# Optimization experiments

Measured on AMD Instinct MI355X. Metric: run time of the kernel, lower is better.

## Reference

```python
import jax, jax.numpy as jnp
import numpy as np

C, PE, L, HEADS = 256, 64, 6, 4
N_GRAPHS, S = 2048, 64            # uniform graphs of S nodes -> dense batch is a reshape
N = N_GRAPHS * S                  # 131072 nodes
E = N * 4                         # 524288 edges
BN_EPS = 1e-5


def _bn(h, g, b):
    # BatchNorm1d, training-mode statistics (biased variance), affine
    m = h.mean(0)
    v = h.var(0)
    return (h - m) / jnp.sqrt(v + BN_EPS) * g + b


def setup_inputs() -> dict:
    key = jax.random.key(0)
    ks = iter(jax.random.split(key, 64))
    def rn(shape, scale=0.05):
        return jax.random.normal(next(ks), shape, dtype=jnp.float32) * scale
    x = jax.random.randint(next(ks), (N, 1), 0, 28)
    pe = jax.random.normal(next(ks), (N, 20), dtype=jnp.float32)
    epg = E // N_GRAPHS
    base = (jnp.arange(E) // epg) * S          # edges stay within their graph
    src = base + jax.random.randint(next(ks), (E,), 0, S)
    dst = base + jax.random.randint(next(ks), (E,), 0, S)
    edge_index = jnp.stack([src, dst])
    edge_attr = jax.random.randint(next(ks), (E,), 0, 4)
    batch = jnp.arange(N) // S
    return dict(
        x=x, pe=pe, edge_index=edge_index, edge_attr=edge_attr, batch=batch,
        node_emb=rn((28, C - PE), 1.0), pe_lin_w=rn((20, PE)), pe_lin_b=jnp.zeros(PE),
        pe_norm_g=jnp.ones(20), pe_norm_b=jnp.zeros(20),
        edge_emb=rn((4, C), 1.0),
        conv_w1=rn((L, C, C)), conv_b1=jnp.zeros((L, C)),
        conv_w2=rn((L, C, C)), conv_b2=jnp.zeros((L, C)),
        attn_in_w=rn((L, C, 3 * C)), attn_in_b=jnp.zeros((L, 3 * C)),
        attn_out_w=rn((L, C, C)), attn_out_b=jnp.zeros((L, C)),
        bn1_g=jnp.ones((L, C)), bn1_b=jnp.zeros((L, C)),
        bn2_g=jnp.ones((L, C)), bn2_b=jnp.zeros((L, C)),
        bn3_g=jnp.ones((L, C)), bn3_b=jnp.zeros((L, C)),
        mlp_w1=rn((L, C, 2 * C)), mlp_b1=jnp.zeros((L, 2 * C)),
        mlp_w2=rn((L, 2 * C, C)), mlp_b2=jnp.zeros((L, C)),
        head_w1=rn((C, C // 2)), head_b1=jnp.zeros(C // 2),
        head_w2=rn((C // 2, C // 4)), head_b2=jnp.zeros(C // 4),
        head_w3=rn((C // 4, 1)), head_b3=jnp.zeros(1),
    )


def reference(x, pe, edge_index, edge_attr, batch, node_emb, pe_lin_w, pe_lin_b,
              pe_norm_g, pe_norm_b, edge_emb, conv_w1, conv_b1, conv_w2, conv_b2,
              attn_in_w, attn_in_b, attn_out_w, attn_out_b,
              bn1_g, bn1_b, bn2_g, bn2_b, bn3_g, bn3_b,
              mlp_w1, mlp_b1, mlp_w2, mlp_b2,
              head_w1, head_b1, head_w2, head_b2, head_w3, head_b3):
    x_pe = _bn(pe, pe_norm_g, pe_norm_b)
    h = jnp.concatenate([node_emb[x[:, 0]], x_pe @ pe_lin_w + pe_lin_b], axis=1)  # [N, C]
    ea = edge_emb[edge_attr]                                                      # [E, C]
    src, dst = edge_index[0], edge_index[1]
    d = C // HEADS
    scale = 1.0 / jnp.sqrt(jnp.float32(d))
    for l in range(L):
        # --- local GINEConv: nn((1+eps)*x_i + sum_j relu(x_j + e_ij)), eps=0 ---
        msg = jax.nn.relu(h[src] + ea)                          # gather + add + relu
        aggr = jax.ops.segment_sum(msg, dst, num_segments=N)    # scatter-add
        z = h + aggr
        hl = jax.nn.relu(z @ conv_w1[l] + conv_b1[l]) @ conv_w2[l] + conv_b2[l]
        hl = _bn(hl + h, bn1_g[l], bn1_b[l])                    # residual + norm1
        # --- global multihead attention on dense batch [G, S, C] ---
        hd = h.reshape(N_GRAPHS, S, C)
        qkv = hd @ attn_in_w[l] + attn_in_b[l]
        q, k, v = jnp.split(qkv, 3, axis=-1)
        q = q.reshape(N_GRAPHS, S, HEADS, d).transpose(0, 2, 1, 3)
        k = k.reshape(N_GRAPHS, S, HEADS, d).transpose(0, 2, 1, 3)
        v = v.reshape(N_GRAPHS, S, HEADS, d).transpose(0, 2, 1, 3)
        a = jax.nn.softmax(jnp.einsum('ghqd,ghkd->ghqk', q, k) * scale, axis=-1)
        o = jnp.einsum('ghqk,ghkd->ghqd', a, v).transpose(0, 2, 1, 3).reshape(N_GRAPHS, S, C)
        o = (o @ attn_out_w[l] + attn_out_b[l]).reshape(N, C)
        ha = _bn(o + h, bn2_g[l], bn2_b[l])                     # residual + norm2
        # --- combine + FFN ---
        out = hl + ha
        ff = jax.nn.relu(out @ mlp_w1[l] + mlp_b1[l]) @ mlp_w2[l] + mlp_b2[l]
        h = _bn(out + ff, bn3_g[l], bn3_b[l])                   # residual + norm3
    pooled = jax.ops.segment_sum(h, batch, num_segments=N_GRAPHS)  # global_add_pool -> [G, C]
    t = jax.nn.relu(pooled @ head_w1 + head_b1)
    t = jax.nn.relu(t @ head_w2 + head_b2)
    return t @ head_w3 + head_b3                                   # [G, 1]
```

## Files before the change

kernel.cpp:

```cpp
#include <hip/hip_runtime.h>

#define N_NODES 131072
#define N_EDGES 524288
#define CCH 256
#define N_GRAPHS_ 2048
#define SEQ 64
#define LAYERS 6

typedef unsigned short US;
typedef __attribute__((ext_vector_type(8))) short v8s;
typedef __attribute__((ext_vector_type(8))) unsigned short v8us;
typedef __attribute__((ext_vector_type(4))) float v4f;

__device__ __forceinline__ float b2f(US u) { return __uint_as_float(((unsigned)u) << 16); }
__device__ __forceinline__ US f2b(float f) {
    unsigned u = __float_as_uint(f);
    return (US)((u + 0x7fff + ((u >> 16) & 1)) >> 16);
}
__device__ __forceinline__ void gload16(const US* g, US* l) {
    __builtin_amdgcn_global_load_lds(
        (const __attribute__((address_space(1))) unsigned int*)g,
        (__attribute__((address_space(3))) unsigned int*)l, 16, 0, 0);
}

__device__ float g_stats[512];
__device__ float g_aff1[512];
__device__ float g_aff2[512];
__device__ float g_aff3[512];
__device__ float g_pe[40];
__device__ float g_peaff[40];
__device__ US    g_wt[6 * 655360];
__device__ int   g_csr[N_EDGES];
__device__ int   g_off[N_GRAPHS_ * 65];

__global__ __launch_bounds__(256) void wt_k(const float* __restrict__ cw1, const float* __restrict__ cw2,
                                            const float* __restrict__ aiw, const float* __restrict__ aow,
                                            const float* __restrict__ mw1, const float* __restrict__ mw2) {
    __shared__ float t[64][65];
    int b = blockIdx.x;
    int l = b / 160, r = b % 160;
    const float* src; int ldw, ldk, ctiles; size_t doff;
    if (r < 16)      { src = cw1 + (size_t)l * 65536;  ldw = 256; ldk = 256; ctiles = 4;  doff = 0;      }
    else if (r < 32) { src = cw2 + (size_t)l * 65536;  ldw = 256; ldk = 256; ctiles = 4;  doff = 65536;  r -= 16; }
    else if (r < 80) { src = aiw + (size_t)l * 196608; ldw = 768; ldk = 256; ctiles = 12; doff = 131072; r -= 32; }
    else if (r < 96) { src = aow + (size_t)l * 65536;  ldw = 256; ldk = 256; ctiles = 4;  doff = 327680; r -= 80; }
    else if (r < 128){ src = mw1 + (size_t)l * 131072; ldw = 512; ldk = 256; ctiles = 8;  doff = 393216; r -= 96; }
    else             { src = mw2 + (size_t)l * 131072; ldw = 256; ldk = 512; ctiles = 4;  doff = 524288; r -= 128; }
    int kt = r / ctiles, ct = r % ctiles;
    int k0 = kt * 64, c0 = ct * 64;
    US* dst = g_wt + (size_t)l * 655360 + doff;
    int tid = threadIdx.x;
    int rr = tid >> 4, c4 = (tid & 15) * 4;
    #pragma unroll
    for (int j = 0; j < 4; j++) {
        float4 v = *(const float4*)(src + (size_t)(k0 + rr + j * 16) * ldw + c0 + c4);
        t[rr + j * 16][c4 + 0] = v.x; t[rr + j * 16][c4 + 1] = v.y;
        t[rr + j * 16][c4 + 2] = v.z; t[rr + j * 16][c4 + 3] = v.w;
    }
    __syncthreads();
    #pragma unroll
    for (int j = 0; j < 4; j++) {
        int crow = rr + j * 16;
        ushort4 o;
        o.x = f2b(t[c4 + 0][crow]); o.y = f2b(t[c4 + 1][crow]);
        o.z = f2b(t[c4 + 2][crow]); o.w = f2b(t[c4 + 3][crow]);
        *(ushort4*)(dst + (size_t)(c0 + crow) * ldk + k0 + c4) = o;
    }
}

__global__ __launch_bounds__(256) void csr_k(const int* __restrict__ ei,
                                             const int* __restrict__ attr) {
    __shared__ int deg[64], off[65];
    int g = blockIdx.x, tid = threadIdx.x;
    if (tid < 64) deg[tid] = 0;
    __syncthreads();
    int e = g * 256 + tid;
    int d = ei[N_EDGES + e] - g * 64;
    int slot = atomicAdd(&deg[d], 1);
    __syncthreads();
    if (tid == 0) {
        off[0] = 0;
        for (int i = 0; i < 64; i++) off[i + 1] = off[i] + deg[i];
    }
    __syncthreads();
    g_csr[g * 256 + off[d] + slot] = (ei[e] - g * 64) | (attr[e] << 6);
    if (tid < 65) g_off[g * 65 + tid] = off[tid];
}

__global__ __launch_bounds__(256) void pe_part_k(const float* __restrict__ pe) {
    __shared__ float red[240], red2[240];
    int b = blockIdx.x, tid = threadIdx.x;
    float s = 0.f, s2 = 0.f;
    if (tid < 240) {
        int ch = tid % 20, sub = tid / 20;
        size_t r0 = (size_t)b * 512;
        for (int r = sub; r < 512; r += 12) {
            float v = pe[(r0 + r) * 20 + ch];
            s += v; s2 += v * v;
        }
        red[tid] = s; red2[tid] = s2;
    }
    __syncthreads();
    if (tid < 20) {
        float ts = 0.f, ts2 = 0.f;
        #pragma unroll
        for (int sub = 0; sub < 12; sub++) { ts += red[sub * 20 + tid]; ts2 += red2[sub * 20 + tid]; }
        atomicAdd(&g_pe[tid], ts);
        atomicAdd(&g_pe[20 + tid], ts2);
    }
}

__global__ __launch_bounds__(64) void pe_fin_k(const float* __restrict__ g,
                                               const float* __restrict__ b) {
    int t = threadIdx.x;
    if (t < 20) {
        float mean = g_pe[t] / (float)N_NODES;
        float var  = g_pe[20 + t] / (float)N_NODES - mean * mean;
        float a = g[t] * rsqrtf(var + 1e-5f);
        g_peaff[t] = a;
        g_peaff[20 + t] = b[t] - mean * a;
        g_pe[t] = 0.f;
        g_pe[20 + t] = 0.f;
    }
}

__global__ __launch_bounds__(256) void embed_k(const int* __restrict__ x,
                                               const float* __restrict__ pe,
                                               const float* __restrict__ node_emb,
                                               const float* __restrict__ plw,
                                               const float* __restrict__ plb,
                                               US* __restrict__ h) {
    int n = blockIdx.x;
    int tid = threadIdx.x;
    int xi = x[n];
    float v;
    if (tid < 192) {
        v = node_emb[xi * 192 + tid];
    } else {
        int j = tid - 192;
        float s = plb[j];
        #pragma unroll
        for (int k = 0; k < 20; k++) {
            float p = pe[(size_t)n * 20 + k] * g_peaff[k] + g_peaff[20 + k];
            s += p * plw[k * 64 + j];
        }
        v = s;
    }
    h[(size_t)n * CCH + tid] = f2b(v);
}

__global__ __launch_bounds__(256) void aggr_z_k(const US* __restrict__ h,
                                                const float* __restrict__ eemb,
                                                US* __restrict__ z) {
    __shared__ US ht[64 * 264];
    __shared__ float em[4 * 260];
    __shared__ int off[65], ce[256];
    int g = blockIdx.x, tid = threadIdx.x;
    for (int v = tid; v < 2048; v += 256) {
        int row = v >> 5, seg = (v & 31) * 8;
        *(v8us*)&ht[row * 264 + seg] = *(const v8us*)(h + (size_t)(g * 64 + row) * 256 + seg);
    }
    for (int i = tid; i < 1024; i += 256)
        em[(i >> 8) * 260 + (i & 255)] = eemb[(i >> 8) * 256 + (i & 255)];
    ce[tid] = g_csr[g * 256 + tid];
    if (tid < 65) off[tid] = g_off[g * 65 + tid];
    __syncthreads();

    int dst = tid >> 2, cq = (tid & 3) * 4;
    float acc[64];
    #pragma unroll
    for (int i = 0; i < 64; i++) acc[i] = 0.f;
    int e1 = off[dst + 1];
    for (int e = off[dst]; e < e1; e++) {
        int val = ce[e];
        int src = val & 63, a = (val >> 6) & 3;
        #pragma unroll
        for (int i = 0; i < 16; i++) {
            int c = cq + i * 16;
            ushort4 hv = *(ushort4*)&ht[src * 264 + c];
            float4 ev = *(float4*)&em[a * 260 + c];
            acc[i * 4 + 0] += fmaxf(b2f(hv.x) + ev.x, 0.f);
            acc[i * 4 + 1] += fmaxf(b2f(hv.y) + ev.y, 0.f);
            acc[i * 4 + 2] += fmaxf(b2f(hv.z) + ev.z, 0.f);
            acc[i * 4 + 3] += fmaxf(b2f(hv.w) + ev.w, 0.f);
        }
    }
    US* zp = z + (size_t)(g * 64 + dst) * 256;
    #pragma unroll
    for (int i = 0; i < 16; i++) {
        int c = cq + i * 16;
        ushort4 hv = *(ushort4*)&ht[dst * 264 + c];
        ushort4 o;
        o.x = f2b(b2f(hv.x) + acc[i * 4 + 0]);
        o.y = f2b(b2f(hv.y) + acc[i * 4 + 1]);
        o.z = f2b(b2f(hv.z) + acc[i * 4 + 2]);
        o.w = f2b(b2f(hv.w) + acc[i * 4 + 3]);
        *(ushort4*)(zp + c) = o;
    }
}

template<int NG, bool STATS>
__global__ __launch_bounds__(256, 4) void gemm_mfma_k(const US* __restrict__ A,
                                                      size_t woff, int ldk,
                                                      int w0, int w1, int w2, int w3,
                                                      const float* __restrict__ bias,
                                                      const US* __restrict__ res,
                                                      US* __restrict__ Y, int mode) {
    const US* __restrict__ Wt = g_wt + woff;
    __shared__ __align__(16) char smem[8192 + 2 * NG * 4096];
    US* As0 = (US*)smem;
    US* As1 = As0 + 2048;
    US* Bs0 = (US*)(smem + 8192);
    US* Bs1 = Bs0 + NG * 2048;
    float* Es = (float*)smem;
    const int NW = NG * 64 + 4;

    int tid = threadIdx.x;
    int bid = blockIdx.x;
    int swz = (bid & 7) * ((int)gridDim.x >> 3) + (bid >> 3);
    size_t row0 = (size_t)swz * 64;
    int w = tid >> 6, l = tid & 63;
    int li = l & 15, hi = l >> 4;
    int sl = hi ^ ((li >> 1) & 3);
    int sr = l >> 2, ss = l & 3;

    int a_off = (w * 16 + li) * 32 + sl * 8;

    v4f acc[NG * 4];
    #pragma unroll
    for (int t = 0; t < NG * 4; t++) acc[t] = (v4f){0.f, 0.f, 0.f, 0.f};

    int ar = w * 16 + sr;
    int akg = (ss ^ ((ar >> 1) & 3)) * 8;
    const US* asrc = A + (row0 + ar) * 256 + akg;

    auto stage = [&](int kc, US* Asb, US* Bsb) {
        int k0 = kc * 32;
        gload16(asrc + k0, Asb + w * 512);
        #pragma unroll
        for (int j = 0; j < NG; j++) {
            int cu = (j * 4 + w) * 16 + sr;
            int grp = cu >> 6;
            int wb = (grp == 0) ? w0 : (grp == 1) ? w1 : (grp == 2) ? w2 : w3;
            int kg = (ss ^ ((cu >> 1) & 3)) * 8;
            gload16(Wt + (size_t)(wb + (cu & 63)) * ldk + k0 + kg,
                    Bsb + (j * 4 + w) * 512);
        }
    };

    stage(0, As0, Bs0);
    __syncthreads();
    for (int kc = 0; kc < 8; kc++) {
        US* Asc = (kc & 1) ? As1 : As0;
        US* Bsc = (kc & 1) ? Bs1 : Bs0;
        if (kc < 7) stage(kc + 1, (kc & 1) ? As0 : As1, (kc & 1) ? Bs0 : Bs1);
        v8s a0 = *(v8s*)(Asc + a_off);
        #pragma unroll
        for (int t = 0; t < NG * 4; t++) {
            v8s bf = *(v8s*)(Bsc + (t * 16 + li) * 32 + sl * 8);
            acc[t] = __builtin_amdgcn_mfma_f32_16x16x32_bf16(a0, bf, acc[t], 0, 0, 0);
        }
        __syncthreads();
    }

    int er_f = tid >> 3;
    int lcb = (tid & 7) * 8;
    float csum = 0.f, csum2 = 0.f;
    #pragma unroll
    for (int p = 0; p < 2; p++) {
        if ((w >> 1) == p) {
            int er0 = (w & 1) * 16 + hi * 4;
            #pragma unroll
            for (int t = 0; t < NG * 4; t++) {
                int grp = t >> 2;
                int wb = (grp == 0) ? w0 : (grp == 1) ? w1 : (grp == 2) ? w2 : w3;
                float bv = bias ? bias[wb + (t & 3) * 16 + li] : 0.f;
                #pragma unroll
                for (int r = 0; r < 4; r++) {
                    float v = acc[t][r] + bv;
                    if (mode == 1) v = fmaxf(v, 0.f);
                    Es[(er0 + r) * NW + t * 16 + li] = v;
                }
            }
        }
        __syncthreads();
        size_t gr = row0 + p * 32 + er_f;
        #pragma unroll
        for (int s = 0; s < NG; s++) {
            int c = s * 64 + lcb;
            float vs[8];
            #pragma unroll
            for (int j = 0; j < 8; j++) vs[j] = Es[er_f * NW + c + j];
            if (mode == 2) {
                v8us rv = *(const v8us*)(res + gr * 256 + c);
                #pragma unroll
                for (int j = 0; j < 8; j++) vs[j] += b2f(rv[j]);
            }
            v8us yv;
            #pragma unroll
            for (int j = 0; j < 8; j++) yv[j] = f2b(vs[j]);
            *(v8us*)(Y + gr * 256 + c) = yv;
            if constexpr (STATS) {
                #pragma unroll
                for (int j = 0; j < 8; j++) Es[er_f * NW + c + j] = vs[j];
            }
        }
        if constexpr (STATS) {
            __syncthreads();
            if (tid < NG * 64) {
                float s1 = 0.f, s2 = 0.f;
                #pragma unroll 8
                for (int r2 = 0; r2 < 32; r2++) {
                    float vv = Es[r2 * NW + tid];
                    s1 += vv; s2 += vv * vv;
                }
                csum += s1; csum2 += s2;
            }
        }
        __syncthreads();
    }
    if constexpr (STATS) {
        if (tid < NG * 64) {
            atomicAdd(&g_stats[tid], csum);
            atomicAdd(&g_stats[CCH + tid], csum2);
        }
    }
}

__global__ __launch_bounds__(64) void attn_k(const US* __restrict__ qkv,
                                             US* __restrict__ o) {
    __shared__ __align__(16) US Ps[64 * 72];
    __shared__ __align__(16) US Vt[64 * 72];
    int g = blockIdx.x, l = threadIdx.x;
    int li = l & 15, hi8 = (l >> 4) * 8, hi4 = (l >> 4) * 4;
    const US* base = qkv + (size_t)g * 64 * 256;

    {
        v8us vv[8];
        #pragma unroll
        for (int jv = 0; jv < 8; jv++)
            vv[jv] = *(const v8us*)(base + l * 256 + 128 + jv * 8);
        #pragma unroll
        for (int jv = 0; jv < 8; jv++)
            #pragma unroll
            for (int e = 0; e < 8; e++)
                Vt[(jv * 8 + e) * 72 + l] = vv[jv][e];
    }

    v8s Qf[4][2], Kf[4][2];
    #pragma unroll
    for (int t = 0; t < 4; t++)
        #pragma unroll
        for (int ds = 0; ds < 2; ds++) {
            Qf[t][ds] = *(const v8s*)(base + (t * 16 + li) * 256 + ds * 32 + hi8);
            Kf[t][ds] = *(const v8s*)(base + (t * 16 + li) * 256 + 64 + ds * 32 + hi8);
        }

    v4f S[4][4];
    #pragma unroll
    for (int qt = 0; qt < 4; qt++)
        #pragma unroll
        for (int kt = 0; kt < 4; kt++) {
            v4f a = (v4f){0.f, 0.f, 0.f, 0.f};
            a = __builtin_amdgcn_mfma_f32_16x16x32_bf16(Qf[qt][0], Kf[kt][0], a, 0, 0, 0);
            a = __builtin_amdgcn_mfma_f32_16x16x32_bf16(Qf[qt][1], Kf[kt][1], a, 0, 0, 0);
            S[qt][kt] = a;
        }

    #pragma unroll
    for (int qt = 0; qt < 4; qt++)
        #pragma unroll
        for (int r = 0; r < 4; r++) {
            float mx = -1e30f;
            #pragma unroll
            for (int kt = 0; kt < 4; kt++) {
                S[qt][kt][r] *= 0.125f;
                mx = fmaxf(mx, S[qt][kt][r]);
            }
            mx = fmaxf(mx, __shfl_xor(mx, 1));
            mx = fmaxf(mx, __shfl_xor(mx, 2));
            mx = fmaxf(mx, __shfl_xor(mx, 4));
            mx = fmaxf(mx, __shfl_xor(mx, 8));
            float sum = 0.f;
            #pragma unroll
            for (int kt = 0; kt < 4; kt++) {
                float e = __expf(S[qt][kt][r] - mx);
                S[qt][kt][r] = e;
                sum += e;
            }
            sum += __shfl_xor(sum, 1);
            sum += __shfl_xor(sum, 2);
            sum += __shfl_xor(sum, 4);
            sum += __shfl_xor(sum, 8);
            float inv = 1.f / sum;
            #pragma unroll
            for (int kt = 0; kt < 4; kt++)
                Ps[(qt * 16 + hi4 + r) * 72 + kt * 16 + li] = f2b(S[qt][kt][r] * inv);
        }

    v4f O[4][4];
    #pragma unroll
    for (int qt = 0; qt < 4; qt++)
        #pragma unroll
        for (int jt = 0; jt < 4; jt++) O[qt][jt] = (v4f){0.f, 0.f, 0.f, 0.f};
    #pragma unroll
    for (int ks = 0; ks < 2; ks++) {
        v8s Pf[4], Vf[4];
        #pragma unroll
        for (int qt = 0; qt < 4; qt++)
            Pf[qt] = *(v8s*)&Ps[(qt * 16 + li) * 72 + ks * 32 + hi8];
        #pragma unroll
        for (int jt = 0; jt < 4; jt++)
            Vf[jt] = *(v8s*)&Vt[(jt * 16 + li) * 72 + ks * 32 + hi8];
        #pragma unroll
        for (int qt = 0; qt < 4; qt++)
            #pragma unroll
            for (int jt = 0; jt < 4; jt++)
                O[qt][jt] = __builtin_amdgcn_mfma_f32_16x16x32_bf16(Pf[qt], Vf[jt], O[qt][jt], 0, 0, 0);
    }

    #pragma unroll
    for (int qt = 0; qt < 4; qt++)
        #pragma unroll
        for (int jt = 0; jt < 4; jt++)
            #pragma unroll
            for (int r = 0; r < 4; r++)
                Ps[(qt * 16 + hi4 + r) * 72 + jt * 16 + li] = f2b(O[qt][jt][r]);
    US* ob = o + (size_t)(g * 64 + l) * 256;
    #pragma unroll
    for (int jv = 0; jv < 8; jv++)
        *(v8us*)(ob + jv * 8) = *(v8us*)&Ps[l * 72 + jv * 8];
}

__global__ __launch_bounds__(256) void affine_k(const float* __restrict__ g,
                                                const float* __restrict__ b, int sel) {
    int c = threadIdx.x;
    float mean = g_stats[c] / (float)N_NODES;
    float var  = g_stats[CCH + c] / (float)N_NODES - mean * mean;
    float a = g[c] * rsqrtf(var + 1e-5f);
    float* dst = (sel == 0) ? g_aff1 : (sel == 1) ? g_aff2 : g_aff3;
    dst[c] = a;
    dst[CCH + c] = b[c] - mean * a;
    g_stats[c] = 0.f;
    g_stats[CCH + c] = 0.f;
}

__global__ __launch_bounds__(256) void combine_k(const US* __restrict__ y1,
                                                 const US* __restrict__ y2,
                                                 US* __restrict__ out) {
    size_t idx = (size_t)blockIdx.x * 256 + threadIdx.x;
    size_t stride = (size_t)gridDim.x * 256;
    for (; idx < (size_t)N_NODES * CCH / 8; idx += stride) {
        size_t i = idx * 8;
        int c = (int)(i & 255);
        v8us a = *(const v8us*)(y1 + i);
        v8us b = *(const v8us*)(y2 + i);
        v8us o;
        #pragma unroll
        for (int j = 0; j < 8; j++) {
            float v = b2f(a[j]) * g_aff1[c + j] + g_aff1[CCH + c + j] +
                      b2f(b[j]) * g_aff2[c + j] + g_aff2[CCH + c + j];
            o[j] = f2b(v);
        }
        *(v8us*)(out + i) = o;
    }
}

__global__ __launch_bounds__(256) void apply_k(US* __restrict__ h) {
    size_t idx = (size_t)blockIdx.x * 256 + threadIdx.x;
    size_t stride = (size_t)gridDim.x * 256;
    for (; idx < (size_t)N_NODES * CCH / 8; idx += stride) {
        size_t i = idx * 8;
        int c = (int)(i & 255);
        v8us a = *(const v8us*)(h + i);
        v8us o;
        #pragma unroll
        for (int j = 0; j < 8; j++)
            o[j] = f2b(b2f(a[j]) * g_aff3[c + j] + g_aff3[CCH + c + j]);
        *(v8us*)(h + i) = o;
    }
}

__global__ __launch_bounds__(256) void pool_k(const US* __restrict__ h,
                                              float* __restrict__ pooled) {
    int g = blockIdx.x, c = threadIdx.x;
    float s = 0.f;
    for (int ss = 0; ss < SEQ; ss++) s += b2f(h[((size_t)g * SEQ + ss) * CCH + c]);
    pooled[(size_t)g * CCH + c] = s;
}

__global__ __launch_bounds__(128) void head_k(const float* __restrict__ pooled,
                                              const float* __restrict__ w1, const float* __restrict__ b1,
                                              const float* __restrict__ w2, const float* __restrict__ b2,
                                              const float* __restrict__ w3, const float* __restrict__ b3,
                                              float* __restrict__ outp) {
    __shared__ float p[256], t1[128], t2[64];
    int g = blockIdx.x, tid = threadIdx.x;
    p[tid] = pooled[(size_t)g * CCH + tid];
    p[tid + 128] = pooled[(size_t)g * CCH + 128 + tid];
    __syncthreads();
    float s = b1[tid];
    for (int k = 0; k < 256; k++) s += p[k] * w1[k * 128 + tid];
    t1[tid] = fmaxf(s, 0.f);
    __syncthreads();
    if (tid < 64) {
        float s2 = b2[tid];
        for (int k = 0; k < 128; k++) s2 += t1[k] * w2[k * 64 + tid];
        t2[tid] = fmaxf(s2, 0.f);
    }
    __syncthreads();
    if (tid == 0) {
        float s3 = b3[0];
        for (int k = 0; k < 64; k++) s3 += t2[k] * w3[k];
        outp[g] = s3;
    }
}

extern "C" void kernel_launch(void* const* d_in, const int* in_sizes, int n_in,
                              void* d_out, int out_size, void* d_ws, size_t ws_size,
                              hipStream_t stream) {
    const int*   x         = (const int*)  d_in[0];
    const float* pe        = (const float*)d_in[1];
    const int*   ei        = (const int*)  d_in[2];
    const int*   eattr     = (const int*)  d_in[3];
    const float* node_emb  = (const float*)d_in[5];
    const float* pe_lin_w  = (const float*)d_in[6];
    const float* pe_lin_b  = (const float*)d_in[7];
    const float* pe_norm_g = (const float*)d_in[8];
    const float* pe_norm_b = (const float*)d_in[9];
    const float* edge_emb  = (const float*)d_in[10];
    const float* conv_w1   = (const float*)d_in[11];
    const float* conv_b1   = (const float*)d_in[12];
    const float* conv_w2   = (const float*)d_in[13];
    const float* conv_b2   = (const float*)d_in[14];
    const float* attn_in_w = (const float*)d_in[15];
    const float* attn_in_b = (const float*)d_in[16];
    const float* attn_out_w= (const float*)d_in[17];
    const float* attn_out_b= (const float*)d_in[18];
    const float* bn1_g     = (const float*)d_in[19];
    const float* bn1_b     = (const float*)d_in[20];
    const float* bn2_g     = (const float*)d_in[21];
    const float* bn2_b     = (const float*)d_in[22];
    const float* bn3_g     = (const float*)d_in[23];
    const float* bn3_b     = (const float*)d_in[24];
    const float* mlp_w1    = (const float*)d_in[25];
    const float* mlp_b1    = (const float*)d_in[26];
    const float* mlp_w2    = (const float*)d_in[27];
    const float* mlp_b2    = (const float*)d_in[28];
    const float* head_w1   = (const float*)d_in[29];
    const float* head_b1   = (const float*)d_in[30];
    const float* head_w2   = (const float*)d_in[31];
    const float* head_b2   = (const float*)d_in[32];
    const float* head_w3   = (const float*)d_in[33];
    const float* head_b3   = (const float*)d_in[34];
    (void)in_sizes; (void)n_in; (void)out_size; (void)ws_size;

    char* ws = (char*)d_ws;
    US* h = (US*)(ws);
    US* A = (US*)(ws + 67108864ULL);
    US* B = (US*)(ws + 134217728ULL);
    US* C = (US*)(ws + 201326592ULL);
    float* pooled = (float*)(ws + 67108864ULL);

    wt_k<<<960, 256, 0, stream>>>(conv_w1, conv_w2, attn_in_w, attn_out_w, mlp_w1, mlp_w2);
    csr_k<<<N_GRAPHS_, 256, 0, stream>>>(ei, eattr);
    pe_part_k<<<256, 256, 0, stream>>>(pe);
    pe_fin_k<<<1, 64, 0, stream>>>(pe_norm_g, pe_norm_b);
    embed_k<<<N_NODES, 256, 0, stream>>>(x, pe, node_emb, pe_lin_w, pe_lin_b, h);

    for (int l = 0; l < LAYERS; l++) {
        size_t wl = (size_t)l * 655360;

        aggr_z_k<<<N_GRAPHS_, 256, 0, stream>>>(h, edge_emb, A);
        gemm_mfma_k<4, false><<<2048, 256, 0, stream>>>(A, wl, 256, 0, 64, 128, 192,
                                                        conv_b1 + l * 256, nullptr, B, 1);
        gemm_mfma_k<4, true><<<2048, 256, 0, stream>>>(B, wl + 65536, 256, 0, 64, 128, 192,
                                                       conv_b2 + l * 256, h, C, 2);
        affine_k<<<1, 256, 0, stream>>>(bn1_g + l * 256, bn1_b + l * 256, 0);

        for (int hh = 0; hh < 4; hh++) {
            gemm_mfma_k<3, false><<<2048, 256, 0, stream>>>(h, wl + 131072, 256,
                                                            hh * 64, 256 + hh * 64, 512 + hh * 64, 0,
                                                            attn_in_b + l * 768, nullptr, A, 0);
            attn_k<<<N_GRAPHS_, 64, 0, stream>>>(A, B + hh * 64);
        }
        gemm_mfma_k<4, true><<<2048, 256, 0, stream>>>(B, wl + 327680, 256, 0, 64, 128, 192,
                                                       attn_out_b + l * 256, h, h, 2);
        affine_k<<<1, 256, 0, stream>>>(bn2_g + l * 256, bn2_b + l * 256, 1);

        combine_k<<<2048, 256, 0, stream>>>(C, h, A);
        gemm_mfma_k<4, false><<<2048, 256, 0, stream>>>(A, wl + 393216, 256, 0, 64, 128, 192,
                                                        mlp_b1 + l * 512, nullptr, B, 1);
        gemm_mfma_k<4, false><<<2048, 256, 0, stream>>>(B, wl + 524288, 512, 0, 64, 128, 192,
                                                        mlp_b2 + l * 256, A, C, 2);
        gemm_mfma_k<4, false><<<2048, 256, 0, stream>>>(A, wl + 393216, 256, 256, 320, 384, 448,
                                                        mlp_b1 + l * 512, nullptr, B, 1);
        gemm_mfma_k<4, true><<<2048, 256, 0, stream>>>(B, wl + 524288 + 256, 512, 0, 64, 128, 192,
                                                       nullptr, C, h, 2);
        affine_k<<<1, 256, 0, stream>>>(bn3_g + l * 256, bn3_b + l * 256, 2);
        apply_k<<<2048, 256, 0, stream>>>(h);
    }

    pool_k<<<N_GRAPHS_, 256, 0, stream>>>(h, pooled);
    head_k<<<N_GRAPHS_, 128, 0, stream>>>(pooled, head_w1, head_b1, head_w2, head_b2,
                                          head_w3, head_b3, (float*)d_out);
}
```

Measured before the change: 5.165 ms.

## Triple-buffer GEMM K-loop with explicit vmcnt waits and separate epilogue buffer

```diff
diff --git a/kernel.cpp b/kernel.cpp
--- a/kernel.cpp
+++ b/kernel.cpp
@@ -200,19 +200,16 @@
 }
 
 template<int NG, bool STATS>
-__global__ __launch_bounds__(256, 4) void gemm_mfma_k(const US* __restrict__ A,
+__global__ __launch_bounds__(256, 2) void gemm_mfma_k(const US* __restrict__ A,
                                                       size_t woff, int ldk,
                                                       int w0, int w1, int w2, int w3,
                                                       const float* __restrict__ bias,
                                                       const US* __restrict__ res,
                                                       US* __restrict__ Y, int mode) {
     const US* __restrict__ Wt = g_wt + woff;
-    __shared__ __align__(16) char smem[8192 + 2 * NG * 4096];
-    US* As0 = (US*)smem;
-    US* As1 = As0 + 2048;
-    US* Bs0 = (US*)(smem + 8192);
-    US* Bs1 = Bs0 + NG * 2048;
-    float* Es = (float*)smem;
+    __shared__ __align__(16) US As0[2048], As1[2048], As2[2048];
+    __shared__ __align__(16) US Bs0[NG * 2048], Bs1[NG * 2048], Bs2[NG * 2048];
+    __shared__ __align__(16) float Es[16 * (NG * 64 + 4)];
     const int NW = NG * 64 + 4;
 
     int tid = threadIdx.x;
@@ -234,7 +231,7 @@
     int akg = (ss ^ ((ar >> 1) & 3)) * 8;
     const US* asrc = A + (row0 + ar) * 256 + akg;
 
-    auto stage = [&](int kc, US* Asb, US* Bsb) {
+    auto stage = [&](int kc, US (&Asb)[2048], US (&Bsb)[NG * 2048]) {
         int k0 = kc * 32;
         gload16(asrc + k0, Asb + w * 512);
         #pragma unroll
@@ -247,29 +244,41 @@
                     Bsb + (j * 4 + w) * 512);
         }
     };
+    auto compute = [&](US (&Asb)[2048], US (&Bsb)[NG * 2048]) {
+        v8s a0 = *(v8s*)(Asb + a_off);
+        #pragma unroll
+        for (int t = 0; t < NG * 4; t++) {
+            v8s bf = *(v8s*)(Bsb + (t * 16 + li) * 32 + sl * 8);
+            acc[t] = __builtin_amdgcn_mfma_f32_16x16x32_bf16(a0, bf, acc[t], 0, 0, 0);
+        }
+    };
+
+    #define WAITS() do { asm volatile("s_waitcnt vmcnt(%0)" :: "n"(NG + 1) : "memory"); \
+                         __builtin_amdgcn_sched_barrier(0); } while (0)
+    #define WAIT0() do { asm volatile("s_waitcnt vmcnt(0)" ::: "memory"); \
+                         __builtin_amdgcn_sched_barrier(0); } while (0)
+    #define BAR() __builtin_amdgcn_s_barrier()
 
     stage(0, As0, Bs0);
-    __syncthreads();
-    for (int kc = 0; kc < 8; kc++) {
-        US* Asc = (kc & 1) ? As1 : As0;
-        US* Bsc = (kc & 1) ? Bs1 : Bs0;
-        if (kc < 7) stage(kc + 1, (kc & 1) ? As0 : As1, (kc & 1) ? Bs0 : Bs1);
-        v8s a0 = *(v8s*)(Asc + a_off);
-        #pragma unroll
-        for (int t = 0; t < NG * 4; t++) {
-            v8s bf = *(v8s*)(Bsc + (t * 16 + li) * 32 + sl * 8);
-            acc[t] = __builtin_amdgcn_mfma_f32_16x16x32_bf16(a0, bf, acc[t], 0, 0, 0);
-        }
+    stage(1, As1, Bs1);
+    WAITS(); BAR();
+    stage(2, As2, Bs2); compute(As0, Bs0); WAITS(); BAR();
+    stage(3, As0, Bs0); compute(As1, Bs1); WAITS(); BAR();
+    stage(4, As1, Bs1); compute(As2, Bs2); WAITS(); BAR();
+    stage(5, As2, Bs2); compute(As0, Bs0); WAITS(); BAR();
+    stage(6, As0, Bs0); compute(As1, Bs1); WAITS(); BAR();
+    stage(7, As1, Bs1); compute(As2, Bs2); WAITS(); BAR();
+    compute(As0, Bs0); WAIT0(); BAR();
+    compute(As1, Bs1);
+    #undef WAITS
+    #undef WAIT0
+    #undef BAR
+
+    float csum = 0.f, csum2 = 0.f;
+    #pragma unroll
+    for (int p = 0; p < 4; p++) {
         __syncthreads();
-    }
-
-    int er_f = tid >> 3;
-    int lcb = (tid & 7) * 8;
-    float csum = 0.f, csum2 = 0.f;
-    #pragma unroll
-    for (int p = 0; p < 2; p++) {
-        if ((w >> 1) == p) {
-            int er0 = (w & 1) * 16 + hi * 4;
+        if (w == p) {
             #pragma unroll
             for (int t = 0; t < NG * 4; t++) {
                 int grp = t >> 2;
@@ -279,18 +288,18 @@
                 for (int r = 0; r < 4; r++) {
                     float v = acc[t][r] + bv;
                     if (mode == 1) v = fmaxf(v, 0.f);
-                    Es[(er0 + r) * NW + t * 16 + li] = v;
+                    Es[(hi * 4 + r) * NW + t * 16 + li] = v;
                 }
             }
         }
         __syncthreads();
-        size_t gr = row0 + p * 32 + er_f;
-        #pragma unroll
-        for (int s = 0; s < NG; s++) {
-            int c = s * 64 + lcb;
+        for (int sidx = tid; sidx < 16 * NG * 8; sidx += 256) {
+            int rr = sidx / (NG * 8);
+            int c = (sidx % (NG * 8)) * 8;
+            size_t gr = row0 + p * 16 + rr;
             float vs[8];
             #pragma unroll
-            for (int j = 0; j < 8; j++) vs[j] = Es[er_f * NW + c + j];
+            for (int j = 0; j < 8; j++) vs[j] = Es[rr * NW + c + j];
             if (mode == 2) {
                 v8us rv = *(const v8us*)(res + gr * 256 + c);
                 #pragma unroll
@@ -302,22 +311,21 @@
             *(v8us*)(Y + gr * 256 + c) = yv;
             if constexpr (STATS) {
                 #pragma unroll
-                for (int j = 0; j < 8; j++) Es[er_f * NW + c + j] = vs[j];
+                for (int j = 0; j < 8; j++) Es[rr * NW + c + j] = vs[j];
             }
         }
         if constexpr (STATS) {
             __syncthreads();
             if (tid < NG * 64) {
                 float s1 = 0.f, s2 = 0.f;
-                #pragma unroll 8
-                for (int r2 = 0; r2 < 32; r2++) {
+                #pragma unroll 4
+                for (int r2 = 0; r2 < 16; r2++) {
                     float vv = Es[r2 * NW + tid];
                     s1 += vv; s2 += vv * vv;
                 }
                 csum += s1; csum2 += s2;
             }
         }
-        __syncthreads();
     }
     if constexpr (STATS) {
         if (tid < NG * 64) {
```

After: 6.734 ms. 30.4% more time.

## Fuse per-head QKV projection GEMM with attention into one kernel

Applied to the files above, without the earlier changes.

```diff
diff --git a/kernel.cpp b/kernel.cpp
--- a/kernel.cpp
+++ b/kernel.cpp
@@ -327,109 +327,175 @@
     }
 }
 
-__global__ __launch_bounds__(64) void attn_k(const US* __restrict__ qkv,
-                                             US* __restrict__ o) {
-    __shared__ __align__(16) US Ps[64 * 72];
-    __shared__ __align__(16) US Vt[64 * 72];
-    int g = blockIdx.x, l = threadIdx.x;
-    int li = l & 15, hi8 = (l >> 4) * 8, hi4 = (l >> 4) * 4;
-    const US* base = qkv + (size_t)g * 64 * 256;
-
+__global__ __launch_bounds__(256, 2) void qkvattn_k(const US* __restrict__ h,
+                                                    size_t woff, int hh,
+                                                    const float* __restrict__ bias,
+                                                    US* __restrict__ o) {
+    const US* __restrict__ Wt = g_wt + woff;
+    __shared__ __align__(16) US As0[2048], As1[2048];
+    __shared__ __align__(16) US Bs0[3 * 2048], Bs1[3 * 2048];
+    __shared__ __align__(16) float Es[16 * 196];
+    __shared__ __align__(16) US Qs[64 * 72];
+    __shared__ __align__(16) US Ks[64 * 72];
+    __shared__ __align__(16) US Vt[64 * 80];
+
+    int tid = threadIdx.x;
+    int bid = blockIdx.x;
+    int g = (bid & 7) * ((int)gridDim.x >> 3) + (bid >> 3);
+    size_t row0 = (size_t)g * 64;
+    int w = tid >> 6, l = tid & 63;
+    int li = l & 15, hi = l >> 4;
+    int sl = hi ^ ((li >> 1) & 3);
+    int sr = l >> 2, ss = l & 3;
+    int w0 = hh * 64, w1 = 256 + hh * 64, w2 = 512 + hh * 64;
+
+    int a_off = (w * 16 + li) * 32 + sl * 8;
+
+    v4f acc[12];
+    #pragma unroll
+    for (int t = 0; t < 12; t++) acc[t] = (v4f){0.f, 0.f, 0.f, 0.f};
+
+    int ar = w * 16 + sr;
+    int akg = (ss ^ ((ar >> 1) & 3)) * 8;
+    const US* asrc = h + (row0 + ar) * 256 + akg;
+
+    auto stage = [&](int kc, US* Asb, US* Bsb) {
+        int k0 = kc * 32;
+        gload16(asrc + k0, Asb + w * 512);
+        #pragma unroll
+        for (int j = 0; j < 3; j++) {
+            int cu = (j * 4 + w) * 16 + sr;
+            int grp = cu >> 6;
+            int wb = (grp == 0) ? w0 : (grp == 1) ? w1 : w2;
+            int kg = (ss ^ ((cu >> 1) & 3)) * 8;
+            gload16(Wt + (size_t)(wb + (cu & 63)) * 256 + k0 + kg,
+                    Bsb + (j * 4 + w) * 512);
+        }
+    };
+
+    stage(0, As0, Bs0);
+    __syncthreads();
+    for (int kc = 0; kc < 8; kc++) {
+        US* Asc = (kc & 1) ? As1 : As0;
+        US* Bsc = (kc & 1) ? Bs1 : Bs0;
+        if (kc < 7) stage(kc + 1, (kc & 1) ? As0 : As1, (kc & 1) ? Bs0 : Bs1);
+        v8s a0 = *(v8s*)(Asc + a_off);
+        #pragma unroll
+        for (int t = 0; t < 12; t++) {
+            v8s bf = *(v8s*)(Bsc + (t * 16 + li) * 32 + sl * 8);
+            acc[t] = __builtin_amdgcn_mfma_f32_16x16x32_bf16(a0, bf, acc[t], 0, 0, 0);
+        }
+        __syncthreads();
+    }
+
+    #pragma unroll
+    for (int p = 0; p < 4; p++) {
+        if (w == p) {
+            #pragma unroll
+            for (int t = 0; t < 12; t++) {
+                int grp = t >> 2;
+                int wb = (grp == 0) ? w0 : (grp == 1) ? w1 : w2;
+                float bv = bias[wb + (t & 3) * 16 + li];
+                #pragma unroll
+                for (int r = 0; r < 4; r++)
+                    Es[(hi * 4 + r) * 196 + t * 16 + li] = acc[t][r] + bv;
+            }
+        }
+        __syncthreads();
+        for (int sidx = tid; sidx < 16 * 24; sidx += 256) {
+            int rr = sidx / 24, cb = (sidx % 24) * 8;
+            int row = p * 16 + rr;
+            if (cb < 128) {
+                v8us v;
+                #pragma unroll
+                for (int j = 0; j < 8; j++) v[j] = f2b(Es[rr * 196 + cb + j]);
+                if (cb < 64) *(v8us*)&Qs[row * 72 + cb] = v;
+                else         *(v8us*)&Ks[row * 72 + cb - 64] = v;
+            } else {
+                #pragma unroll
+                for (int j = 0; j < 8; j++)
+                    Vt[(cb - 128 + j) * 80 + row] = f2b(Es[rr * 196 + cb + j]);
+            }
+        }
+        __syncthreads();
+    }
+
+    int hi8 = hi * 8, hi4 = hi * 4;
+    v8s Qf[2], Kf[4][2];
+    #pragma unroll
+    for (int ds = 0; ds < 2; ds++)
+        Qf[ds] = *(v8s*)&Qs[(w * 16 + li) * 72 + ds * 32 + hi8];
+    #pragma unroll
+    for (int kt = 0; kt < 4; kt++)
+        #pragma unroll
+        for (int ds = 0; ds < 2; ds++)
+            Kf[kt][ds] = *(v8s*)&Ks[(kt * 16 + li) * 72 + ds * 32 + hi8];
+    __syncthreads();
+
+    v4f S[4];
+    #pragma unroll
+    for (int kt = 0; kt < 4; kt++) {
+        v4f a = (v4f){0.f, 0.f, 0.f, 0.f};
+        a = __builtin_amdgcn_mfma_f32_16x16x32_bf16(Qf[0], Kf[kt][0], a, 0, 0, 0);
+        a = __builtin_amdgcn_mfma_f32_16x16x32_bf16(Qf[1], Kf[kt][1], a, 0, 0, 0);
+        S[kt] = a;
+    }
+    #pragma unroll
+    for (int r = 0; r < 4; r++) {
+        float mx = -1e30f;
+        #pragma unroll
+        for (int kt = 0; kt < 4; kt++) {
+            S[kt][r] *= 0.125f;
+            mx = fmaxf(mx, S[kt][r]);
+        }
+        mx = fmaxf(mx, __shfl_xor(mx, 1));
+        mx = fmaxf(mx, __shfl_xor(mx, 2));
+        mx = fmaxf(mx, __shfl_xor(mx, 4));
+        mx = fmaxf(mx, __shfl_xor(mx, 8));
+        float sum = 0.f;
+        #pragma unroll
+        for (int kt = 0; kt < 4; kt++) {
+            float e = __expf(S[kt][r] - mx);
+            S[kt][r] = e;
+            sum += e;
+        }
+        sum += __shfl_xor(sum, 1);
+        sum += __shfl_xor(sum, 2);
+        sum += __shfl_xor(sum, 4);
+        sum += __shfl_xor(sum, 8);
+        float inv = 1.f / sum;
+        #pragma unroll
+        for (int kt = 0; kt < 4; kt++)
+            Qs[(w * 16 + hi4 + r) * 72 + kt * 16 + li] = f2b(S[kt][r] * inv);
+    }
+    __syncthreads();
+
+    v4f O[4];
+    #pragma unroll
+    for (int jt = 0; jt < 4; jt++) O[jt] = (v4f){0.f, 0.f, 0.f, 0.f};
+    #pragma unroll
+    for (int ks = 0; ks < 2; ks++) {
+        v8s Pf = *(v8s*)&Qs[(w * 16 + li) * 72 + ks * 32 + hi8];
+        #pragma unroll
+        for (int jt = 0; jt < 4; jt++) {
+            v8s Vf = *(v8s*)&Vt[(jt * 16 + li) * 80 + ks * 32 + hi8];
+            O[jt] = __builtin_amdgcn_mfma_f32_16x16x32_bf16(Pf, Vf, O[jt], 0, 0, 0);
+        }
+    }
+    __syncthreads();
+    #pragma unroll
+    for (int jt = 0; jt < 4; jt++)
+        #pragma unroll
+        for (int r = 0; r < 4; r++)
+            Qs[(w * 16 + hi4 + r) * 72 + jt * 16 + li] = f2b(O[jt][r]);
+    __syncthreads();
     {
-        v8us vv[8];
-        #pragma unroll
-        for (int jv = 0; jv < 8; jv++)
-            vv[jv] = *(const v8us*)(base + l * 256 + 128 + jv * 8);
-        #pragma unroll
-        for (int jv = 0; jv < 8; jv++)
-            #pragma unroll
-            for (int e = 0; e < 8; e++)
-                Vt[(jv * 8 + e) * 72 + l] = vv[jv][e];
-    }
-
-    v8s Qf[4][2], Kf[4][2];
-    #pragma unroll
-    for (int t = 0; t < 4; t++)
-        #pragma unroll
-        for (int ds = 0; ds < 2; ds++) {
-            Qf[t][ds] = *(const v8s*)(base + (t * 16 + li) * 256 + ds * 32 + hi8);
-            Kf[t][ds] = *(const v8s*)(base + (t * 16 + li) * 256 + 64 + ds * 32 + hi8);
-        }
-
-    v4f S[4][4];
-    #pragma unroll
-    for (int qt = 0; qt < 4; qt++)
-        #pragma unroll
-        for (int kt = 0; kt < 4; kt++) {
-            v4f a = (v4f){0.f, 0.f, 0.f, 0.f};
-            a = __builtin_amdgcn_mfma_f32_16x16x32_bf16(Qf[qt][0], Kf[kt][0], a, 0, 0, 0);
-            a = __builtin_amdgcn_mfma_f32_16x16x32_bf16(Qf[qt][1], Kf[kt][1], a, 0, 0, 0);
-            S[qt][kt] = a;
-        }
-
-    #pragma unroll
-    for (int qt = 0; qt < 4; qt++)
-        #pragma unroll
-        for (int r = 0; r < 4; r++) {
-            float mx = -1e30f;
-            #pragma unroll
-            for (int kt = 0; kt < 4; kt++) {
-                S[qt][kt][r] *= 0.125f;
-                mx = fmaxf(mx, S[qt][kt][r]);
-            }
-            mx = fmaxf(mx, __shfl_xor(mx, 1));
-            mx = fmaxf(mx, __shfl_xor(mx, 2));
-            mx = fmaxf(mx, __shfl_xor(mx, 4));
-            mx = fmaxf(mx, __shfl_xor(mx, 8));
-            float sum = 0.f;
-            #pragma unroll
-            for (int kt = 0; kt < 4; kt++) {
-                float e = __expf(S[qt][kt][r] - mx);
-                S[qt][kt][r] = e;
-                sum += e;
-            }
-            sum += __shfl_xor(sum, 1);
-            sum += __shfl_xor(sum, 2);
-            sum += __shfl_xor(sum, 4);
-            sum += __shfl_xor(sum, 8);
-            float inv = 1.f / sum;
-            #pragma unroll
-            for (int kt = 0; kt < 4; kt++)
-                Ps[(qt * 16 + hi4 + r) * 72 + kt * 16 + li] = f2b(S[qt][kt][r] * inv);
-        }
-
-    v4f O[4][4];
-    #pragma unroll
-    for (int qt = 0; qt < 4; qt++)
-        #pragma unroll
-        for (int jt = 0; jt < 4; jt++) O[qt][jt] = (v4f){0.f, 0.f, 0.f, 0.f};
-    #pragma unroll
-    for (int ks = 0; ks < 2; ks++) {
-        v8s Pf[4], Vf[4];
-        #pragma unroll
-        for (int qt = 0; qt < 4; qt++)
-            Pf[qt] = *(v8s*)&Ps[(qt * 16 + li) * 72 + ks * 32 + hi8];
-        #pragma unroll
-        for (int jt = 0; jt < 4; jt++)
-            Vf[jt] = *(v8s*)&Vt[(jt * 16 + li) * 72 + ks * 32 + hi8];
-        #pragma unroll
-        for (int qt = 0; qt < 4; qt++)
-            #pragma unroll
-            for (int jt = 0; jt < 4; jt++)
-                O[qt][jt] = __builtin_amdgcn_mfma_f32_16x16x32_bf16(Pf[qt], Vf[jt], O[qt][jt], 0, 0, 0);
-    }
-
-    #pragma unroll
-    for (int qt = 0; qt < 4; qt++)
-        #pragma unroll
-        for (int jt = 0; jt < 4; jt++)
-            #pragma unroll
-            for (int r = 0; r < 4; r++)
-                Ps[(qt * 16 + hi4 + r) * 72 + jt * 16 + li] = f2b(O[qt][jt][r]);
-    US* ob = o + (size_t)(g * 64 + l) * 256;
-    #pragma unroll
-    for (int jv = 0; jv < 8; jv++)
-        *(v8us*)(ob + jv * 8) = *(v8us*)&Ps[l * 72 + jv * 8];
+        int row = tid >> 2, cq = (tid & 3) * 16;
+        v8us o0 = *(v8us*)&Qs[row * 72 + cq];
+        v8us o1 = *(v8us*)&Qs[row * 72 + cq + 8];
+        *(v8us*)(o + (row0 + row) * 256 + cq) = o0;
+        *(v8us*)(o + (row0 + row) * 256 + cq + 8) = o1;
+    }
 }
 
 __global__ __launch_bounds__(256) void affine_k(const float* __restrict__ g,
@@ -578,12 +644,9 @@
                                                        conv_b2 + l * 256, h, C, 2);
         affine_k<<<1, 256, 0, stream>>>(bn1_g + l * 256, bn1_b + l * 256, 0);
 
-        for (int hh = 0; hh < 4; hh++) {
-            gemm_mfma_k<3, false><<<2048, 256, 0, stream>>>(h, wl + 131072, 256,
-                                                            hh * 64, 256 + hh * 64, 512 + hh * 64, 0,
-                                                            attn_in_b + l * 768, nullptr, A, 0);
-            attn_k<<<N_GRAPHS_, 64, 0, stream>>>(A, B + hh * 64);
-        }
+        for (int hh = 0; hh < 4; hh++)
+            qkvattn_k<<<2048, 256, 0, stream>>>(h, wl + 131072, hh,
+                                                attn_in_b + l * 768, B + hh * 64);
         gemm_mfma_k<4, true><<<2048, 256, 0, stream>>>(B, wl + 327680, 256, 0, 64, 128, 192,
                                                        attn_out_b + l * 256, h, h, 2);
         affine_k<<<1, 256, 0, stream>>>(bn2_g + l * 256, bn2_b + l * 256, 1);
```

Measured after the change: 6.273 ms. 1.21x slower.

## Fuse two-layer GEMM pairs into one kernel keeping hidden activations in LDS

Applied to the files above, without the earlier changes.

```diff
diff --git a/kernel.cpp b/kernel.cpp
--- a/kernel.cpp
+++ b/kernel.cpp
@@ -325,6 +325,175 @@
             atomicAdd(&g_stats[CCH + tid], csum2);
         }
     }
+}
+
+template<int NH>
+__global__ __launch_bounds__(256, 2) void mlp_fused_k(const US* __restrict__ A,
+                                                      size_t woff1, const float* __restrict__ bias1,
+                                                      size_t woff2, int ldk2,
+                                                      const float* __restrict__ bias2,
+                                                      const US* __restrict__ res,
+                                                      US* __restrict__ Y) {
+    const US* __restrict__ W1t = g_wt + woff1;
+    const US* __restrict__ W2t = g_wt + woff2;
+    __shared__ __align__(16) char smem[73728];
+    US* As0 = (US*)smem;
+    US* As1 = (US*)(smem + 4096);
+    US* Bs0 = (US*)(smem + 8192);
+    US* Bs1 = (US*)(smem + 24576);
+    float* Es = (float*)smem;
+    US* Ts = (US*)(smem + 40960);
+
+    int tid = threadIdx.x;
+    int bid = blockIdx.x;
+    int swz = (bid & 7) * ((int)gridDim.x >> 3) + (bid >> 3);
+    size_t row0 = (size_t)swz * 64;
+    int w = tid >> 6, l = tid & 63;
+    int li = l & 15, hi = l >> 4;
+    int sl = hi ^ ((li >> 1) & 3);
+    int sr = l >> 2, ss = l & 3;
+
+    int a_off = (w * 16 + li) * 32 + sl * 8;
+
+    v4f accY[16];
+    #pragma unroll
+    for (int t = 0; t < 16; t++) accY[t] = (v4f){0.f, 0.f, 0.f, 0.f};
+
+    int ar = w * 16 + sr;
+    int akg = (ss ^ ((ar >> 1) & 3)) * 8;
+    const US* asrc = A + (row0 + ar) * 256 + akg;
+
+    #pragma unroll
+    for (int q = 0; q < NH; q++) {
+        v4f accT[16];
+        #pragma unroll
+        for (int t = 0; t < 16; t++) accT[t] = (v4f){0.f, 0.f, 0.f, 0.f};
+
+        auto stageA = [&](int kc, US* Asb, US* Bsb) {
+            int k0 = kc * 32;
+            gload16(asrc + k0, Asb + w * 512);
+            #pragma unroll
+            for (int j = 0; j < 4; j++) {
+                int cu = (j * 4 + w) * 16 + sr;
+                int kg = (ss ^ ((cu >> 1) & 3)) * 8;
+                gload16(W1t + (size_t)(q * 256 + cu) * 256 + k0 + kg,
+                        Bsb + (j * 4 + w) * 512);
+            }
+        };
+        stageA(0, As0, Bs0);
+        __syncthreads();
+        for (int kc = 0; kc < 8; kc++) {
+            US* Asc = (kc & 1) ? As1 : As0;
+            US* Bsc = (kc & 1) ? Bs1 : Bs0;
+            if (kc < 7) stageA(kc + 1, (kc & 1) ? As0 : As1, (kc & 1) ? Bs0 : Bs1);
+            v8s a0 = *(v8s*)(Asc + a_off);
+            #pragma unroll
+            for (int t = 0; t < 16; t++) {
+                v8s bf = *(v8s*)(Bsc + (t * 16 + li) * 32 + sl * 8);
+                accT[t] = __builtin_amdgcn_mfma_f32_16x16x32_bf16(a0, bf, accT[t], 0, 0, 0);
+            }
+            __syncthreads();
+        }
+        #pragma unroll
+        for (int p = 0; p < 2; p++) {
+            if ((w >> 1) == p) {
+                int er0 = (w & 1) * 16 + hi * 4;
+                #pragma unroll
+                for (int t = 0; t < 16; t++) {
+                    float bv = bias1[q * 256 + t * 16 + li];
+                    #pragma unroll
+                    for (int r = 0; r < 4; r++)
+                        Es[(er0 + r) * 260 + t * 16 + li] = fmaxf(accT[t][r] + bv, 0.f);
+                }
+            }
+            __syncthreads();
+            {
+                int er = tid >> 3, lcb = (tid & 7) * 8;
+                int rowL = p * 32 + er;
+                int rsw = (rowL >> 1) & 3;
+                #pragma unroll
+                for (int s = 0; s < 4; s++) {
+                    int col = s * 64 + lcb;
+                    v8us tv;
+                    #pragma unroll
+                    for (int j = 0; j < 8; j++) tv[j] = f2b(Es[er * 260 + col + j]);
+                    int chunk = col >> 5, slot = ((col >> 3) & 3) ^ rsw;
+                    *(v8us*)&Ts[chunk * 2048 + rowL * 32 + slot * 8] = tv;
+                }
+            }
+            __syncthreads();
+        }
+        auto stageB = [&](int kc, US* Bsb) {
+            int k0 = q * 256 + kc * 32;
+            #pragma unroll
+            for (int j = 0; j < 4; j++) {
+                int cu = (j * 4 + w) * 16 + sr;
+                int kg = (ss ^ ((cu >> 1) & 3)) * 8;
+                gload16(W2t + (size_t)cu * ldk2 + k0 + kg, Bsb + (j * 4 + w) * 512);
+            }
+        };
+        stageB(0, Bs0);
+        __syncthreads();
+        for (int kc = 0; kc < 8; kc++) {
+            US* Bsc = (kc & 1) ? Bs1 : Bs0;
+            if (kc < 7) stageB(kc + 1, (kc & 1) ? Bs0 : Bs1);
+            v8s a0 = *(v8s*)(Ts + kc * 2048 + a_off);
+            #pragma unroll
+            for (int t = 0; t < 16; t++) {
+                v8s bf = *(v8s*)(Bsc + (t * 16 + li) * 32 + sl * 8);
+                accY[t] = __builtin_amdgcn_mfma_f32_16x16x32_bf16(a0, bf, accY[t], 0, 0, 0);
+            }
+            __syncthreads();
+        }
+    }
+
+    int er_f = tid >> 3;
+    int lcb = (tid & 7) * 8;
+    float csum = 0.f, csum2 = 0.f;
+    #pragma unroll
+    for (int p = 0; p < 2; p++) {
+        if ((w >> 1) == p) {
+            int er0 = (w & 1) * 16 + hi * 4;
+            #pragma unroll
+            for (int t = 0; t < 16; t++) {
+                float bv = bias2[t * 16 + li];
+                #pragma unroll
+                for (int r = 0; r < 4; r++)
+                    Es[(er0 + r) * 260 + t * 16 + li] = accY[t][r] + bv;
+            }
+        }
+        __syncthreads();
+        size_t gr = row0 + p * 32 + er_f;
+        #pragma unroll
+        for (int s = 0; s < 4; s++) {
+            int c = s * 64 + lcb;
+            float vs[8];
+            #pragma unroll
+            for (int j = 0; j < 8; j++) vs[j] = Es[er_f * 260 + c + j];
+            v8us rv = *(const v8us*)(res + gr * 256 + c);
+            #pragma unroll
+            for (int j = 0; j < 8; j++) vs[j] += b2f(rv[j]);
+            v8us yv;
+            #pragma unroll
+            for (int j = 0; j < 8; j++) yv[j] = f2b(vs[j]);
+            *(v8us*)(Y + gr * 256 + c) = yv;
+            #pragma unroll
+            for (int j = 0; j < 8; j++) Es[er_f * 260 + c + j] = vs[j];
+        }
+        __syncthreads();
+        {
+            float s1 = 0.f, s2 = 0.f;
+            #pragma unroll 8
+            for (int r2 = 0; r2 < 32; r2++) {
+                float vv = Es[r2 * 260 + tid];
+                s1 += vv; s2 += vv * vv;
+            }
+            csum += s1; csum2 += s2;
+        }
+        __syncthreads();
+    }
+    atomicAdd(&g_stats[tid], csum);
+    atomicAdd(&g_stats[CCH + tid], csum2);
 }
 
 __global__ __launch_bounds__(64) void attn_k(const US* __restrict__ qkv,
@@ -572,10 +741,9 @@
         size_t wl = (size_t)l * 655360;
 
         aggr_z_k<<<N_GRAPHS_, 256, 0, stream>>>(h, edge_emb, A);
-        gemm_mfma_k<4, false><<<2048, 256, 0, stream>>>(A, wl, 256, 0, 64, 128, 192,
-                                                        conv_b1 + l * 256, nullptr, B, 1);
-        gemm_mfma_k<4, true><<<2048, 256, 0, stream>>>(B, wl + 65536, 256, 0, 64, 128, 192,
-                                                       conv_b2 + l * 256, h, C, 2);
+        mlp_fused_k<1><<<2048, 256, 0, stream>>>(A, wl, conv_b1 + l * 256,
+                                                 wl + 65536, 256, conv_b2 + l * 256,
+                                                 h, C);
         affine_k<<<1, 256, 0, stream>>>(bn1_g + l * 256, bn1_b + l * 256, 0);
 
         for (int hh = 0; hh < 4; hh++) {
@@ -589,14 +757,9 @@
         affine_k<<<1, 256, 0, stream>>>(bn2_g + l * 256, bn2_b + l * 256, 1);
 
         combine_k<<<2048, 256, 0, stream>>>(C, h, A);
-        gemm_mfma_k<4, false><<<2048, 256, 0, stream>>>(A, wl + 393216, 256, 0, 64, 128, 192,
-                                                        mlp_b1 + l * 512, nullptr, B, 1);
-        gemm_mfma_k<4, false><<<2048, 256, 0, stream>>>(B, wl + 524288, 512, 0, 64, 128, 192,
-                                                        mlp_b2 + l * 256, A, C, 2);
-        gemm_mfma_k<4, false><<<2048, 256, 0, stream>>>(A, wl + 393216, 256, 256, 320, 384, 448,
-                                                        mlp_b1 + l * 512, nullptr, B, 1);
-        gemm_mfma_k<4, true><<<2048, 256, 0, stream>>>(B, wl + 524288 + 256, 512, 0, 64, 128, 192,
-                                                       nullptr, C, h, 2);
+        mlp_fused_k<2><<<2048, 256, 0, stream>>>(A, wl + 393216, mlp_b1 + l * 512,
+                                                 wl + 524288, 512, mlp_b2 + l * 256,
+                                                 A, h);
         affine_k<<<1, 256, 0, stream>>>(bn3_g + l * 256, bn3_b + l * 256, 2);
         apply_k<<<2048, 256, 0, stream>>>(h);
     }
```

Result: no change. 5.097 ms (-1.3%).
